# Kernel optimization log

Hardware: AMD Instinct MI355X
Metric: run time of the kernel (lower is better)

## Reference

```python
import jax, jax.numpy as jnp
import numpy as np

ALPHA, BETA, GAMMA, EPS = 10.0, 0.1, 1.0, 1e-20
MARK_INDEX = jnp.array([0, 29, 88, 117])

B, S, D, P, C, V = 64, 128, 2048, 118, 2, 512


def setup_inputs() -> dict:
    key = jax.random.key(0)
    ks = jax.random.split(key, 9)
    qy_raw = jax.random.uniform(ks[4], (B, S, V), dtype=jnp.float32)
    qy = qy_raw / jnp.sum(qy_raw, axis=-1, keepdims=True)  # probabilities
    return {
        "zs": jax.random.normal(ks[0], (B, S, D), dtype=jnp.float32),
        "rzs": jax.random.normal(ks[1], (B, S, D), dtype=jnp.float32),
        "pts": jax.random.normal(ks[2], (B, S, P, C), dtype=jnp.float32),
        "pts_gt": jax.random.normal(ks[3], (B, S, P, C), dtype=jnp.float32),
        "qy": qy,
        "logits": jax.random.normal(ks[5], (B, S, V), dtype=jnp.float32),
        "best": jax.random.normal(ks[6], (B, P, C), dtype=jnp.float32),
        "best_gt": jax.random.normal(ks[7], (B, P, C), dtype=jnp.float32),
        "mapping": jax.random.randint(ks[8], (B, S), 0, S, dtype=jnp.int64),
        "vector_dims": V,
    }


def _mse(a, b):
    return jnp.mean(jnp.square(a - b))


def reference(zs, rzs, pts, pts_gt, qy, logits, best, best_gt, mapping, vector_dims):
    # KL divergence vs uniform categorical over vector_dims
    log_g = jnp.log(jnp.float32(1.0) / vector_dims)
    kld = jnp.mean(jnp.sum(qy * (jnp.log(qy + EPS) - log_g), axis=-1))

    best_pts_loss = _mse(best, best_gt) + ALPHA * _mse(
        best[..., MARK_INDEX, :], best_gt[..., MARK_INDEX, :]
    )

    # mapping-indexed gather along dim 1 (vectorized form of the double loop;
    # per-element mse means are all over equal-sized slices, so the summed/
    # averaged loop equals a single global mean over the gathered tensors)
    rz_m = jnp.take_along_axis(rzs, mapping[:, :, None], axis=1)          # [B,S,D]
    x_m = jnp.take_along_axis(pts, mapping[:, :, None, None], axis=1)    # [B,S,P,C]
    recon = _mse(rz_m, zs)
    disk = _mse(x_m, pts_gt)
    landmark = _mse(x_m[..., MARK_INDEX, :], pts_gt[..., MARK_INDEX, :])
    pts_loss = disk + ALPHA * landmark

    total = BETA * kld + GAMMA * recon + pts_loss + best_pts_loss
    return total
```

## Files before the change

kernel.cpp:

```cpp
#include <hip/hip_runtime.h>
#include <math.h>

#define NB 64
#define NS 128
#define ND 2048
#define NP 118
#define NC 2
#define NV 512

constexpr int SEG0 = (NB * NS * ND) / 4;
constexpr int SEG1 = (NB * NS * NV) / 4;
constexpr int SEG2 = (NB * NS * NP * NC) / 4;
constexpr int SEG3 = (NB * NP * NC) / 4;

constexpr int RECON_BLOCKS = 4096;
constexpr int KLD_BLOCKS   = 512;
constexpr int PTS_BLOCKS   = 512;
constexpr int BEST_BLOCKS  = 16;
constexpr int TOTAL_BLOCKS = RECON_BLOCKS + KLD_BLOCKS + PTS_BLOCKS + BEST_BLOCKS;

__global__ __launch_bounds__(256) void cqloss_kernel(
    const float* __restrict__ zs, const float* __restrict__ rzs,
    const float* __restrict__ pts, const float* __restrict__ pts_gt,
    const float* __restrict__ qy,
    const float* __restrict__ best, const float* __restrict__ best_gt,
    const int* __restrict__ mapping, const int* __restrict__ vd,
    float* __restrict__ out)
{
    const float w_recon = 1.0f / 16777216.0f;
    const float w_kld   = 0.1f / 8192.0f;
    const float w_disk  = 1.0f / 1933312.0f;
    const float w_land  = 10.0f / 65536.0f;
    const float w_best  = 1.0f / 15104.0f;
    const float w_bland = 10.0f / 512.0f;

    const int t   = threadIdx.x;
    const int blk = blockIdx.x;
    float acc = 0.0f;

    __shared__ int mrow[16];

    if (blk < RECON_BLOCKS) {
        const int row0 = blk << 1;
        const int m0 = mapping[row0];
        const int m1 = mapping[row0 + 1];
        const int b0 = row0 >> 7;
        const int b1 = (row0 + 1) >> 7;
        const float4* zp0 = (const float4*)(zs  + ((size_t)row0 << 11));
        const float4* zp1 = (const float4*)(zs  + ((size_t)(row0 + 1) << 11));
        const float4* rp0 = (const float4*)(rzs + ((size_t)((b0 << 7) + m0) << 11));
        const float4* rp1 = (const float4*)(rzs + ((size_t)((b1 << 7) + m1) << 11));
        float4 za = zp0[t], zb = zp0[t + 256];
        float4 ra = rp0[t], rb = rp0[t + 256];
        float4 zc = zp1[t], zd = zp1[t + 256];
        float4 rc = rp1[t], rd = rp1[t + 256];
        float s = 0.0f;
        {
            float dx = ra.x - za.x, dy = ra.y - za.y, dz = ra.z - za.z, dw = ra.w - za.w;
            s += dx*dx + dy*dy + dz*dz + dw*dw;
        }
        {
            float dx = rb.x - zb.x, dy = rb.y - zb.y, dz = rb.z - zb.z, dw = rb.w - zb.w;
            s += dx*dx + dy*dy + dz*dz + dw*dw;
        }
        {
            float dx = rc.x - zc.x, dy = rc.y - zc.y, dz = rc.z - zc.z, dw = rc.w - zc.w;
            s += dx*dx + dy*dy + dz*dz + dw*dw;
        }
        {
            float dx = rd.x - zd.x, dy = rd.y - zd.y, dz = rd.z - zd.z, dw = rd.w - zd.w;
            s += dx*dx + dy*dy + dz*dz + dw*dw;
        }
        acc = w_recon * s;
    } else if (blk < RECON_BLOCKS + KLD_BLOCKS) {
        const int rb = blk - RECON_BLOCKS;
        const float log_g = -__logf((float)vd[0]);
        const float4* qp = (const float4*)qy + ((size_t)rb << 11) + t;
        float4 q[8];
        #pragma unroll
        for (int k = 0; k < 8; ++k) q[k] = qp[k * 256];
        float s = 0.0f;
        #pragma unroll
        for (int k = 0; k < 8; ++k) {
            s += q[k].x * (__logf(q[k].x + 1e-20f) - log_g)
               + q[k].y * (__logf(q[k].y + 1e-20f) - log_g)
               + q[k].z * (__logf(q[k].z + 1e-20f) - log_g)
               + q[k].w * (__logf(q[k].w + 1e-20f) - log_g);
        }
        acc = w_kld * s;
    } else if (blk < RECON_BLOCKS + KLD_BLOCKS + PTS_BLOCKS) {
        const int rb = blk - (RECON_BLOCKS + KLD_BLOCKS);
        if (t < 16) mrow[t] = mapping[(rb << 4) + t];
        __syncthreads();
        const int bs_base = rb << 4;
        #pragma unroll
        for (int j = 0; j < 3; ++j) {
            const int w = t + j * 256;
            const unsigned rl = (unsigned)w / 59u;
            const int qo = w - (int)rl * 59;
            const int bs = bs_base + (int)rl;
            const int b  = bs >> 7;
            const int m  = mrow[rl];
            const float4 x = *(const float4*)(pts    + ((size_t)((b << 7) + m) * 236 + (qo << 2)));
            const float4 g = *(const float4*)(pts_gt + ((size_t)(rb * 944 + w) << 2));
            const float* xp = (const float*)&x;
            const float* gp = (const float*)&g;
            const int p2 = qo << 1;
            #pragma unroll
            for (int jj = 0; jj < 4; ++jj) {
                const int p = p2 + (jj >> 1);
                const bool marked = (p == 0) | (p == 29) | (p == 88) | (p == 117);
                const float wgt = w_disk + (marked ? w_land : 0.0f);
                const float d = xp[jj] - gp[jj];
                acc += wgt * d * d;
            }
        }
        {
            const int w = t + 768;
            if (w < 944) {
                const unsigned rl = (unsigned)w / 59u;
                const int qo = w - (int)rl * 59;
                const int bs = bs_base + (int)rl;
                const int b  = bs >> 7;
                const int m  = mrow[rl];
                const float4 x = *(const float4*)(pts    + ((size_t)((b << 7) + m) * 236 + (qo << 2)));
                const float4 g = *(const float4*)(pts_gt + ((size_t)(rb * 944 + w) << 2));
                const float* xp = (const float*)&x;
                const float* gp = (const float*)&g;
                const int p2 = qo << 1;
                #pragma unroll
                for (int jj = 0; jj < 4; ++jj) {
                    const int p = p2 + (jj >> 1);
                    const bool marked = (p == 0) | (p == 29) | (p == 88) | (p == 117);
                    const float wgt = w_disk + (marked ? w_land : 0.0f);
                    const float d = xp[jj] - gp[jj];
                    acc += wgt * d * d;
                }
            }
        }
    } else {
        const int db = blk - (RECON_BLOCKS + KLD_BLOCKS + PTS_BLOCKS);
        if (t < 236) {
            const int l = db * 236 + t;
            const unsigned bq = (unsigned)l / 59u;
            const int qo = l - (int)bq * 59;
            const float4 x = *(const float4*)(best    + ((size_t)l << 2));
            const float4 g = *(const float4*)(best_gt + ((size_t)l << 2));
            const float* xp = (const float*)&x;
            const float* gp = (const float*)&g;
            const int p2 = qo << 1;
            #pragma unroll
            for (int jj = 0; jj < 4; ++jj) {
                const int p = p2 + (jj >> 1);
                const bool marked = (p == 0) | (p == 29) | (p == 88) | (p == 117);
                const float wgt = w_best + (marked ? w_bland : 0.0f);
                const float d = xp[jj] - gp[jj];
                acc += wgt * d * d;
            }
        }
    }

    #pragma unroll
    for (int o = 32; o > 0; o >>= 1) acc += __shfl_down(acc, o, 64);

    __shared__ float wsum[4];
    const int lane = t & 63;
    const int wave = t >> 6;
    if (lane == 0) wsum[wave] = acc;
    __syncthreads();
    if (t == 0) {
        atomicAdd(out, wsum[0] + wsum[1] + wsum[2] + wsum[3]);
    }
}

extern "C" void kernel_launch(void* const* d_in, const int* in_sizes, int n_in,
                              void* d_out, int out_size, void* d_ws, size_t ws_size,
                              hipStream_t stream) {
    const float* zs      = (const float*)d_in[0];
    const float* rzs     = (const float*)d_in[1];
    const float* pts     = (const float*)d_in[2];
    const float* pts_gt  = (const float*)d_in[3];
    const float* qy      = (const float*)d_in[4];
    const float* best    = (const float*)d_in[6];
    const float* best_gt = (const float*)d_in[7];
    const int*   mapping = (const int*)d_in[8];
    const int*   vd      = (const int*)d_in[9];
    float* out = (float*)d_out;

    hipMemsetAsync(out, 0, sizeof(float), stream);

    cqloss_kernel<<<TOTAL_BLOCKS, 256, 0, stream>>>(zs, rzs, pts, pts_gt, qy,
                                                    best, best_gt, mapping, vd, out);
}
```

Measured before the change: 214.9 us.

## Replace global atomics with per-block partials and a reduce kernel; widen recon blocks

Each block now writes its partial sum to workspace instead of doing an atomicAdd on one output float, and a second single-block kernel sums the partials. This drops the memset and the atomic contention on the output. Recon blocks now handle four rows each (half as many blocks), with all loads issued before any arithmetic. The pts branch is restructured so its four loads are issued together using predication. The cost is an extra kernel launch and a dependence on workspace.

```diff
diff --git a/kernel.cpp b/kernel.cpp
--- a/kernel.cpp
+++ b/kernel.cpp
@@ -8,24 +8,19 @@
 #define NC 2
 #define NV 512
 
-constexpr int SEG0 = (NB * NS * ND) / 4;
-constexpr int SEG1 = (NB * NS * NV) / 4;
-constexpr int SEG2 = (NB * NS * NP * NC) / 4;
-constexpr int SEG3 = (NB * NP * NC) / 4;
-
-constexpr int RECON_BLOCKS = 4096;
+constexpr int RECON_BLOCKS = 2048;
 constexpr int KLD_BLOCKS   = 512;
 constexpr int PTS_BLOCKS   = 512;
 constexpr int BEST_BLOCKS  = 16;
 constexpr int TOTAL_BLOCKS = RECON_BLOCKS + KLD_BLOCKS + PTS_BLOCKS + BEST_BLOCKS;
 
-__global__ __launch_bounds__(256) void cqloss_kernel(
+__global__ __launch_bounds__(256) void cq_main(
     const float* __restrict__ zs, const float* __restrict__ rzs,
     const float* __restrict__ pts, const float* __restrict__ pts_gt,
     const float* __restrict__ qy,
     const float* __restrict__ best, const float* __restrict__ best_gt,
     const int* __restrict__ mapping, const int* __restrict__ vd,
-    float* __restrict__ out)
+    float* __restrict__ partials)
 {
     const float w_recon = 1.0f / 16777216.0f;
     const float w_kld   = 0.1f / 8192.0f;
@@ -41,34 +36,31 @@
     __shared__ int mrow[16];
 
     if (blk < RECON_BLOCKS) {
-        const int row0 = blk << 1;
-        const int m0 = mapping[row0];
-        const int m1 = mapping[row0 + 1];
-        const int b0 = row0 >> 7;
-        const int b1 = (row0 + 1) >> 7;
-        const float4* zp0 = (const float4*)(zs  + ((size_t)row0 << 11));
-        const float4* zp1 = (const float4*)(zs  + ((size_t)(row0 + 1) << 11));
-        const float4* rp0 = (const float4*)(rzs + ((size_t)((b0 << 7) + m0) << 11));
-        const float4* rp1 = (const float4*)(rzs + ((size_t)((b1 << 7) + m1) << 11));
-        float4 za = zp0[t], zb = zp0[t + 256];
-        float4 ra = rp0[t], rb = rp0[t + 256];
-        float4 zc = zp1[t], zd = zp1[t + 256];
-        float4 rc = rp1[t], rd = rp1[t + 256];
+        const int r0 = blk << 2;
+        const int b  = r0 >> 7;
+        const int m0 = mapping[r0];
+        const int m1 = mapping[r0 + 1];
+        const int m2 = mapping[r0 + 2];
+        const int m3 = mapping[r0 + 3];
+        const float4* zb4 = (const float4*)zs  + ((size_t)r0 << 9);
+        const float4* rz4 = (const float4*)rzs + ((size_t)b << 16);
+        const int rowbase0 = m0 << 9, rowbase1 = m1 << 9, rowbase2 = m2 << 9, rowbase3 = m3 << 9;
+        float4 z[8], r[8];
+        #pragma unroll
+        for (int k = 0; k < 8; ++k) z[k] = zb4[t + (k << 8)];
+        r[0] = rz4[rowbase0 + t];
+        r[1] = rz4[rowbase0 + 256 + t];
+        r[2] = rz4[rowbase1 + t];
+        r[3] = rz4[rowbase1 + 256 + t];
+        r[4] = rz4[rowbase2 + t];
+        r[5] = rz4[rowbase2 + 256 + t];
+        r[6] = rz4[rowbase3 + t];
+        r[7] = rz4[rowbase3 + 256 + t];
         float s = 0.0f;
-        {
-            float dx = ra.x - za.x, dy = ra.y - za.y, dz = ra.z - za.z, dw = ra.w - za.w;
-            s += dx*dx + dy*dy + dz*dz + dw*dw;
-        }
-        {
-            float dx = rb.x - zb.x, dy = rb.y - zb.y, dz = rb.z - zb.z, dw = rb.w - zb.w;
-            s += dx*dx + dy*dy + dz*dz + dw*dw;
-        }
-        {
-            float dx = rc.x - zc.x, dy = rc.y - zc.y, dz = rc.z - zc.z, dw = rc.w - zc.w;
-            s += dx*dx + dy*dy + dz*dz + dw*dw;
-        }
-        {
-            float dx = rd.x - zd.x, dy = rd.y - zd.y, dz = rd.z - zd.z, dw = rd.w - zd.w;
+        #pragma unroll
+        for (int k = 0; k < 8; ++k) {
+            float dx = r[k].x - z[k].x, dy = r[k].y - z[k].y;
+            float dz = r[k].z - z[k].z, dw = r[k].w - z[k].w;
             s += dx*dx + dy*dy + dz*dz + dw*dw;
         }
         acc = w_recon * s;
@@ -93,49 +85,36 @@
         if (t < 16) mrow[t] = mapping[(rb << 4) + t];
         __syncthreads();
         const int bs_base = rb << 4;
+        float4 x[4], g[4];
+        int pbase[4];
         #pragma unroll
-        for (int j = 0; j < 3; ++j) {
+        for (int j = 0; j < 4; ++j) {
             const int w = t + j * 256;
             const unsigned rl = (unsigned)w / 59u;
             const int qo = w - (int)rl * 59;
-            const int bs = bs_base + (int)rl;
+            const bool valid = (w < 944);
+            const int rl_c = valid ? (int)rl : 0;
+            const int bs = bs_base + rl_c;
             const int b  = bs >> 7;
-            const int m  = mrow[rl];
-            const float4 x = *(const float4*)(pts    + ((size_t)((b << 7) + m) * 236 + (qo << 2)));
-            const float4 g = *(const float4*)(pts_gt + ((size_t)(rb * 944 + w) << 2));
-            const float* xp = (const float*)&x;
-            const float* gp = (const float*)&g;
-            const int p2 = qo << 1;
+            const int m  = mrow[rl_c];
+            const size_t xi = (size_t)((b << 7) + m) * 236 + (qo << 2);
+            const size_t gi = (size_t)(rb * 944 + w) << 2;
+            pbase[j] = qo << 1;
+            x[j] = valid ? *(const float4*)(pts    + xi) : make_float4(0,0,0,0);
+            g[j] = valid ? *(const float4*)(pts_gt + gi) : make_float4(0,0,0,0);
+            if (!valid) pbase[j] = -100;
+        }
+        #pragma unroll
+        for (int j = 0; j < 4; ++j) {
+            const float* xp = (const float*)&x[j];
+            const float* gp = (const float*)&g[j];
             #pragma unroll
             for (int jj = 0; jj < 4; ++jj) {
-                const int p = p2 + (jj >> 1);
+                const int p = pbase[j] + (jj >> 1);
                 const bool marked = (p == 0) | (p == 29) | (p == 88) | (p == 117);
                 const float wgt = w_disk + (marked ? w_land : 0.0f);
                 const float d = xp[jj] - gp[jj];
                 acc += wgt * d * d;
-            }
-        }
-        {
-            const int w = t + 768;
-            if (w < 944) {
-                const unsigned rl = (unsigned)w / 59u;
-                const int qo = w - (int)rl * 59;
-                const int bs = bs_base + (int)rl;
-                const int b  = bs >> 7;
-                const int m  = mrow[rl];
-                const float4 x = *(const float4*)(pts    + ((size_t)((b << 7) + m) * 236 + (qo << 2)));
-                const float4 g = *(const float4*)(pts_gt + ((size_t)(rb * 944 + w) << 2));
-                const float* xp = (const float*)&x;
-                const float* gp = (const float*)&g;
-                const int p2 = qo << 1;
-                #pragma unroll
-                for (int jj = 0; jj < 4; ++jj) {
-                    const int p = p2 + (jj >> 1);
-                    const bool marked = (p == 0) | (p == 29) | (p == 88) | (p == 117);
-                    const float wgt = w_disk + (marked ? w_land : 0.0f);
-                    const float d = xp[jj] - gp[jj];
-                    acc += wgt * d * d;
-                }
             }
         }
     } else {
@@ -168,9 +147,21 @@
     const int wave = t >> 6;
     if (lane == 0) wsum[wave] = acc;
     __syncthreads();
-    if (t == 0) {
-        atomicAdd(out, wsum[0] + wsum[1] + wsum[2] + wsum[3]);
-    }
+    if (t == 0) partials[blk] = wsum[0] + wsum[1] + wsum[2] + wsum[3];
+}
+
+__global__ __launch_bounds__(256) void cq_reduce(
+    const float* __restrict__ partials, float* __restrict__ out)
+{
+    const int t = threadIdx.x;
+    float acc = 0.0f;
+    for (int i = t; i < TOTAL_BLOCKS; i += 256) acc += partials[i];
+    #pragma unroll
+    for (int o = 32; o > 0; o >>= 1) acc += __shfl_down(acc, o, 64);
+    __shared__ float wsum[4];
+    if ((t & 63) == 0) wsum[t >> 6] = acc;
+    __syncthreads();
+    if (t == 0) out[0] = wsum[0] + wsum[1] + wsum[2] + wsum[3];
 }
 
 extern "C" void kernel_launch(void* const* d_in, const int* in_sizes, int n_in,
@@ -185,10 +176,10 @@
     const float* best_gt = (const float*)d_in[7];
     const int*   mapping = (const int*)d_in[8];
     const int*   vd      = (const int*)d_in[9];
-    float* out = (float*)d_out;
+    float* out      = (float*)d_out;
+    float* partials = (float*)d_ws;
 
-    hipMemsetAsync(out, 0, sizeof(float), stream);
-
-    cqloss_kernel<<<TOTAL_BLOCKS, 256, 0, stream>>>(zs, rzs, pts, pts_gt, qy,
-                                                    best, best_gt, mapping, vd, out);
+    cq_main<<<TOTAL_BLOCKS, 256, 0, stream>>>(zs, rzs, pts, pts_gt, qy,
+                                              best, best_gt, mapping, vd, partials);
+    cq_reduce<<<1, 256, 0, stream>>>(partials, out);
 }
```

Result: faster. 190.2 us (-11.5%).
